# Performance work log

Hardware: AMD Instinct MI355X
Metric: run time of the kernel (lower is better)

Reference implementation:

```python
import jax, jax.numpy as jnp
import numpy as np

N_CRD = 32   # ceil(0.5 * 64) coordinate features
K = 16       # clus_val for knn
EPS = 1e-12


def _masked_dist(coords, mask):
    """Pairwise euclidean distances with padded/self pairs set to +inf.
    coords: [B,N,D], mask: [B,N] bool. Returns dist [B,N,N], valid [B,N,N]."""
    sq = jnp.sum(coords * coords, axis=-1)                 # [B,N]
    gram = jnp.einsum('bnd,bmd->bnm', coords, coords)      # [B,N,N]
    d2 = sq[:, :, None] + sq[:, None, :] - 2.0 * gram
    dist = jnp.sqrt(jnp.clip(d2, EPS, None))
    eye = jnp.eye(dist.shape[-1], dtype=bool)
    valid = (mask[:, :, None] & mask[:, None, :]) & ~eye   # fc adjmat, no self-loops
    dist = jnp.where(valid, dist, jnp.inf)                 # pad_val = +inf for eucl
    return dist, valid


def _knn(dist, k):
    """Boolean adjacency: True for the k smallest distances per row."""
    _, idx = jax.lax.top_k(-dist, k)                       # [B,N,K] nearest neighbours
    B, N, _ = dist.shape
    b = jnp.arange(B)[:, None, None]
    n = jnp.arange(N)[None, :, None]
    return jnp.zeros((B, N, N), bool).at[b, n, idx].set(True)


def setup_inputs() -> dict:
    key = jax.random.key(0)
    k1, k2 = jax.random.split(key)
    B, N, F = 64, 1024, 64
    nodes = jax.random.normal(k1, (B, N, F), jnp.float32)
    # realistic ragged graphs: each graph has between N/2 and N valid nodes
    lengths = jax.random.randint(k2, (B,), N // 2, N + 1)
    mask = jnp.arange(N)[None, :] < lengths[:, None]       # [B,N] bool
    return {"nodes": nodes, "mask": mask}


def reference(nodes, mask):
    coords = nodes[..., :N_CRD]
    dist, valid = _masked_dist(coords, mask)
    adjmat = _knn(dist, K) & valid                         # drop padded/self picks
    # dense analogue of distmat[new_adjmat].unsqueeze(-1): zeros off the adjacency
    new_edges = jnp.where(adjmat[..., None], dist[..., None], 0.0)  # [B,N,N,1]
    return new_edges, adjmat
```

## Files before the change

### kernel.cpp

```cpp
#include <hip/hip_runtime.h>
#include <math.h>

#define NROW 1024
#define INF_BITS 0x7F800000u
#define WINDOW   4.0e-3f
#define CLAMP_EPS 1e-12f

typedef float nf4 __attribute__((ext_vector_type(4)));

__device__ __forceinline__ unsigned long long ull_min(unsigned long long a, unsigned long long b) {
    return a < b ? a : b;
}
__device__ __forceinline__ unsigned umax2(unsigned a, unsigned b) { return a > b ? a : b; }

#define ROW_MINMAX(K, MN, MX)                                                           \
    {                                                                                   \
        MN = 0xFFFFFFFFu; MX = 0u;                                                      \
        _Pragma("unroll")                                                               \
        for (int tt = 0; tt < 16; ++tt) {                                               \
            const unsigned kk_ = K[tt];                                                 \
            MN = kk_ < MN ? kk_ : MN;                                                   \
            const unsigned kf_ = (kk_ < INF_BITS) ? kk_ : 0u;                           \
            MX = kf_ > MX ? kf_ : MX;                                                   \
        }                                                                               \
        _Pragma("unroll")                                                               \
        for (int d = 1; d < 64; d <<= 1) {                                              \
            const unsigned omn = (unsigned)__shfl_xor((int)MN, d);                      \
            const unsigned omx = (unsigned)__shfl_xor((int)MX, d);                      \
            MN = omn < MN ? omn : MN;                                                   \
            MX = omx > MX ? omx : MX;                                                   \
        }                                                                               \
    }

#define BISECT_STEP(K, LO, HI)                                                          \
    {                                                                                   \
        const unsigned mid_ = LO + ((HI - LO) >> 1);                                    \
        int cnt_ = 0;                                                                   \
        _Pragma("unroll")                                                               \
        for (int tt = 0; tt < 16; ++tt)                                                 \
            cnt_ += __popcll(__ballot(K[tt] < mid_));                                   \
        if (cnt_ >= 16) HI = mid_; else LO = mid_;                                      \
    }

#define RESOLVE_ROW(K, V, RLOC, SELOUT)                                                 \
    {                                                                                   \
        const float Vw = __uint_as_float(V) + WINDOW;                                   \
        int cS = 0, nE = 0, cW = 0;                                                     \
        unsigned ltm = 0u, eqm = 0u, cm = 0u;                                           \
        _Pragma("unroll")                                                               \
        for (int tt = 0; tt < 16; ++tt) {                                               \
            const unsigned kk_ = K[tt];                                                 \
            const bool l_ = kk_ < (V);                                                  \
            const bool e_ = kk_ == (V);                                                 \
            const bool c_ = __uint_as_float(kk_) <= Vw;                                 \
            cS += __popcll(__ballot(l_));                                               \
            nE += __popcll(__ballot(e_));                                               \
            cW += __popcll(__ballot(c_));                                               \
            ltm |= (l_ ? 1u : 0u) << tt;                                                \
            eqm |= (e_ ? 1u : 0u) << tt;                                                \
            cm  |= (c_ ? 1u : 0u) << tt;                                                \
        }                                                                               \
        if (cS + nE == 16 && cW == 16) {                                                \
            SELOUT = ltm | eqm;                                                         \
        } else {                                                                        \
            int myj = -1;                                                               \
            {                                                                           \
                int cum = 0;                                                            \
                _Pragma("unroll")                                                       \
                for (int tt = 0; tt < 16; ++tt) {                                       \
                    const unsigned long long bm = __ballot((cm >> tt) & 1u);            \
                    const int pc = __popcll(bm);                                        \
                    if (myj < 0 && lane >= cum && lane < cum + pc) {                    \
                        unsigned long long mm = bm;                                     \
                        for (int z = lane - cum; z > 0; --z) mm &= mm - 1ull;           \
                        myj = tt * 64 + (__ffsll((unsigned long long)mm) - 1);          \
                    }                                                                   \
                    cum += pc;                                                          \
                }                                                                       \
            }                                                                           \
            unsigned long long dbits = ~0ull;                                           \
            if (myj >= 0) {                                                             \
                const float4* cp = (const float4*)(nbase + (size_t)myj * 64);           \
                double sq_ = 0.0, dt_ = 0.0;                                            \
                _Pragma("unroll")                                                       \
                for (int f = 0; f < 8; ++f) {                                           \
                    const float4 v = cp[f];                                             \
                    const float4 a = rowc[(RLOC) * 8 + f];                              \
                    sq_ = fma((double)v.x, (double)v.x, sq_);                           \
                    sq_ = fma((double)v.y, (double)v.y, sq_);                           \
                    sq_ = fma((double)v.z, (double)v.z, sq_);                           \
                    sq_ = fma((double)v.w, (double)v.w, sq_);                           \
                    dt_ = fma((double)v.x, (double)a.x, dt_);                           \
                    dt_ = fma((double)v.y, (double)a.y, dt_);                           \
                    dt_ = fma((double)v.z, (double)a.z, dt_);                           \
                    dt_ = fma((double)v.w, (double)a.w, dt_);                           \
                }                                                                       \
                double d64 = fma(-2.0, dt_, sqr64[RLOC] + sq_);                         \
                d64 = fmax(d64, (double)CLAMP_EPS);                                     \
                dbits = (unsigned long long)__double_as_longlong(d64);                  \
            }                                                                           \
            unsigned selb = 0u;                                                         \
            bool act = (myj >= 0);                                                      \
            for (int round = 0; round < 16; ++round) {                                  \
                unsigned long long best = act ? dbits : ~0ull;                          \
                _Pragma("unroll")                                                       \
                for (int d = 1; d < 64; d <<= 1)                                        \
                    best = ull_min(best,                                                \
                        (unsigned long long)__shfl_xor((long long)best, d));            \
                int pj = (act && dbits == best) ? myj : 0x7FFFFFFF;                     \
                _Pragma("unroll")                                                       \
                for (int d = 1; d < 64; d <<= 1) {                                      \
                    const int o = __shfl_xor(pj, d);                                    \
                    pj = o < pj ? o : pj;                                               \
                }                                                                       \
                if (myj == pj) act = false;                                             \
                if (lane == (pj & 63)) selb |= 1u << (pj >> 6);                         \
            }                                                                           \
            SELOUT = selb;                                                              \
        }                                                                               \
    }

__global__ __launch_bounds__(256) void transpose_norm_kernel(
    const float* __restrict__ nodes, float4* __restrict__ wsT,
    float* __restrict__ sqc)
{
    const int w = blockIdx.x;
    const int l = (w & 7) * 32 + (w >> 3);
    const int g = l * 256 + threadIdx.x;
    const int b = g >> 10, j = g & 1023;
    const float4* cp = (const float4*)(nodes + (size_t)g * 64);
    float4 c[8];
    float s = 0.f;
#pragma unroll
    for (int f = 0; f < 8; ++f) {
        c[f] = cp[f];
        s = fmaf(c[f].x, c[f].x, s); s = fmaf(c[f].y, c[f].y, s);
        s = fmaf(c[f].z, c[f].z, s); s = fmaf(c[f].w, c[f].w, s);
    }
#pragma unroll
    for (int f = 0; f < 8; ++f)
        wsT[(((size_t)b * 8 + f) << 10) + j] = c[f];
    sqc[g] = s;
}

template <int USE_WS>
__global__ __launch_bounds__(64) void edge_knn_kernel(
    const float* __restrict__ nodes,
    const int*   __restrict__ mask,
    const float4* __restrict__ wsT,
    const float* __restrict__ sqcw,
    float*       __restrict__ out)
{
    const int lane = threadIdx.x;
    const int blk  = (int)((blockIdx.x & 7) * 2048 + (blockIdx.x >> 3));
    const int b    = blk >> 8;
    const int rowbase = (blk & 255) * 4;

    const int* maskb = mask + b * NROW;
    float* edges = out + (size_t)b * NROW * NROW;
    float* adjm  = out + (size_t)64 * NROW * NROW + (size_t)b * NROW * NROW;

    const int anyv = maskb[rowbase] | maskb[rowbase + 1] | maskb[rowbase + 2] | maskb[rowbase + 3];
    if (!anyv) {
        const nf4 z = {0.f, 0.f, 0.f, 0.f};
#pragma unroll
        for (int r = 0; r < 4; ++r) {
            nf4* e4 = reinterpret_cast<nf4*>(edges + (size_t)(rowbase + r) * NROW);
            nf4* a4 = reinterpret_cast<nf4*>(adjm  + (size_t)(rowbase + r) * NROW);
#pragma unroll
            for (int q = 0; q < 4; ++q) {
                __builtin_nontemporal_store(z, e4 + q * 64 + lane);
                __builtin_nontemporal_store(z, a4 + q * 64 + lane);
            }
        }
        return;
    }

    __shared__ float4 rowc[4 * 8];
    __shared__ float  sqr32s[4];
    __shared__ double sqr64[4];

    const float* nbase = nodes + (size_t)b * NROW * 64;

    if (lane < 32) {
        const int r = lane >> 3, f = lane & 7;
        rowc[lane] = ((const float4*)(nbase + (size_t)(rowbase + r) * 64))[f];
    }
    __syncthreads();
    if (lane < 4) {
        double s = 0.0;
#pragma unroll
        for (int f = 0; f < 8; ++f) {
            const float4 v = rowc[lane * 8 + f];
            s = fma((double)v.x, (double)v.x, s);
            s = fma((double)v.y, (double)v.y, s);
            s = fma((double)v.z, (double)v.z, s);
            s = fma((double)v.w, (double)v.w, s);
        }
        sqr64[lane] = s;
        sqr32s[lane] = (float)s;
    }
    __syncthreads();

    unsigned mb = 0u;
#pragma unroll
    for (int tt = 0; tt < 16; ++tt)
        mb |= (maskb[tt * 64 + lane] != 0 ? 1u : 0u) << tt;

    const int row0 = rowbase;
    const bool rv0 = maskb[row0 + 0] != 0;
    const bool rv1 = maskb[row0 + 1] != 0;
    const bool rv2 = maskb[row0 + 2] != 0;
    const bool rv3 = maskb[row0 + 3] != 0;
    const float sqr0 = sqr32s[0], sqr1 = sqr32s[1];
    const float sqr2 = sqr32s[2], sqr3 = sqr32s[3];

    unsigned k0[16], k1[16], k2[16], k3[16];

#pragma unroll
    for (int tt = 0; tt < 16; ++tt) {
        const int j = tt * 64 + lane;
        float4 c[8];
        float sA;
        if (USE_WS) {
            const float4* tbase = wsT + ((size_t)b * 8 << 10);
#pragma unroll
            for (int f = 0; f < 8; ++f) c[f] = tbase[(f << 10) + j];
            sA = sqcw[(size_t)b * NROW + j];
        } else {
            const float4* cp = (const float4*)(nbase + (size_t)j * 64);
#pragma unroll
            for (int f = 0; f < 8; ++f) c[f] = cp[f];
            sA = 0.f;
#pragma unroll
            for (int f = 0; f < 8; ++f) {
                sA = fmaf(c[f].x, c[f].x, sA); sA = fmaf(c[f].y, c[f].y, sA);
                sA = fmaf(c[f].z, c[f].z, sA); sA = fmaf(c[f].w, c[f].w, sA);
            }
        }

        float d0 = 0.f, d1 = 0.f, d2 = 0.f, d3 = 0.f;
#pragma unroll
        for (int f = 0; f < 8; ++f) {
            const float4 v  = c[f];
            const float4 a0 = rowc[0 * 8 + f];
            const float4 a1 = rowc[1 * 8 + f];
            const float4 a2 = rowc[2 * 8 + f];
            const float4 a3 = rowc[3 * 8 + f];
            d0 = fmaf(v.x, a0.x, d0); d0 = fmaf(v.y, a0.y, d0);
            d0 = fmaf(v.z, a0.z, d0); d0 = fmaf(v.w, a0.w, d0);
            d1 = fmaf(v.x, a1.x, d1); d1 = fmaf(v.y, a1.y, d1);
            d1 = fmaf(v.z, a1.z, d1); d1 = fmaf(v.w, a1.w, d1);
            d2 = fmaf(v.x, a2.x, d2); d2 = fmaf(v.y, a2.y, d2);
            d2 = fmaf(v.z, a2.z, d2); d2 = fmaf(v.w, a2.w, d2);
            d3 = fmaf(v.x, a3.x, d3); d3 = fmaf(v.y, a3.y, d3);
            d3 = fmaf(v.z, a3.z, d3); d3 = fmaf(v.w, a3.w, d3);
        }

        const bool cv = (mb >> tt) & 1u;
        float e_;
        e_ = fmaxf(fmaf(-2.f, d0, sqr0 + sA), CLAMP_EPS);
        k0[tt] = (cv && j != row0 + 0) ? __float_as_uint(e_) : INF_BITS;
        e_ = fmaxf(fmaf(-2.f, d1, sqr1 + sA), CLAMP_EPS);
        k1[tt] = (cv && j != row0 + 1) ? __float_as_uint(e_) : INF_BITS;
        e_ = fmaxf(fmaf(-2.f, d2, sqr2 + sA), CLAMP_EPS);
        k2[tt] = (cv && j != row0 + 2) ? __float_as_uint(e_) : INF_BITS;
        e_ = fmaxf(fmaf(-2.f, d3, sqr3 + sA), CLAMP_EPS);
        k3[tt] = (cv && j != row0 + 3) ? __float_as_uint(e_) : INF_BITS;
    }

    unsigned mn0, mx0, mn1, mx1, mn2, mx2, mn3, mx3;
    ROW_MINMAX(k0, mn0, mx0);
    ROW_MINMAX(k1, mn1, mx1);
    ROW_MINMAX(k2, mn2, mx2);
    ROW_MINMAX(k3, mn3, mx3);

    unsigned lo0 = mn0, hi0 = mx0 + 1u;
    unsigned lo1 = mn1, hi1 = mx1 + 1u;
    unsigned lo2 = mn2, hi2 = mx2 + 1u;
    unsigned lo3 = mn3, hi3 = mx3 + 1u;
    if (!rv0) { lo0 = 0u; hi0 = 1u; }
    if (!rv1) { lo1 = 0u; hi1 = 1u; }
    if (!rv2) { lo2 = 0u; hi2 = 1u; }
    if (!rv3) { lo3 = 0u; hi3 = 1u; }

    for (;;) {
        const unsigned dm = umax2(umax2(hi0 - lo0, hi1 - lo1), umax2(hi2 - lo2, hi3 - lo3));
        if (dm <= 1u) break;
        BISECT_STEP(k0, lo0, hi0);
        BISECT_STEP(k1, lo1, hi1);
        BISECT_STEP(k2, lo2, hi2);
        BISECT_STEP(k3, lo3, hi3);
    }

    unsigned sel0 = 0u, sel1 = 0u, sel2 = 0u, sel3 = 0u;
    if (rv0) RESOLVE_ROW(k0, lo0, 0, sel0);
    if (rv1) RESOLVE_ROW(k1, lo1, 1, sel1);
    if (rv2) RESOLVE_ROW(k2, lo2, 2, sel2);
    if (rv3) RESOLVE_ROW(k3, lo3, 3, sel3);

#pragma unroll
    for (int tt = 0; tt < 16; ++tt) {
        const int j = tt * 64 + lane;
        {
            const bool s = (sel0 >> tt) & 1u;
            __builtin_nontemporal_store(s ? sqrtf(__uint_as_float(k0[tt])) : 0.f,
                                        edges + (size_t)(row0 + 0) * NROW + j);
            __builtin_nontemporal_store(s ? 1.f : 0.f,
                                        adjm + (size_t)(row0 + 0) * NROW + j);
        }
        {
            const bool s = (sel1 >> tt) & 1u;
            __builtin_nontemporal_store(s ? sqrtf(__uint_as_float(k1[tt])) : 0.f,
                                        edges + (size_t)(row0 + 1) * NROW + j);
            __builtin_nontemporal_store(s ? 1.f : 0.f,
                                        adjm + (size_t)(row0 + 1) * NROW + j);
        }
        {
            const bool s = (sel2 >> tt) & 1u;
            __builtin_nontemporal_store(s ? sqrtf(__uint_as_float(k2[tt])) : 0.f,
                                        edges + (size_t)(row0 + 2) * NROW + j);
            __builtin_nontemporal_store(s ? 1.f : 0.f,
                                        adjm + (size_t)(row0 + 2) * NROW + j);
        }
        {
            const bool s = (sel3 >> tt) & 1u;
            __builtin_nontemporal_store(s ? sqrtf(__uint_as_float(k3[tt])) : 0.f,
                                        edges + (size_t)(row0 + 3) * NROW + j);
            __builtin_nontemporal_store(s ? 1.f : 0.f,
                                        adjm + (size_t)(row0 + 3) * NROW + j);
        }
    }
}

extern "C" void kernel_launch(void* const* d_in, const int* in_sizes, int n_in,
                              void* d_out, int out_size, void* d_ws, size_t ws_size,
                              hipStream_t stream)
{
    const float* nodes = (const float*)d_in[0];
    const int*   mask  = (const int*)d_in[1];
    float* out = (float*)d_out;

    dim3 grid(64 * 256);
    dim3 block(64);

    const size_t wsT_f4 = (size_t)64 * 8 * 1024;
    const size_t need   = wsT_f4 * sizeof(float4) + (size_t)64 * NROW * sizeof(float);
    const bool   use_ws = ws_size >= need;

    if (use_ws) {
        float4* wsT = (float4*)d_ws;
        float*  sqc = (float*)((char*)d_ws + wsT_f4 * sizeof(float4));
        hipLaunchKernelGGL(transpose_norm_kernel, dim3(64 * NROW / 256), dim3(256), 0, stream,
                           nodes, wsT, sqc);
        hipLaunchKernelGGL((edge_knn_kernel<1>), grid, block, 0, stream,
                           nodes, mask, (const float4*)wsT, (const float*)sqc, out);
    } else {
        hipLaunchKernelGGL((edge_knn_kernel<0>), grid, block, 0, stream,
                           nodes, mask, (const float4*)nullptr, (const float*)nullptr, out);
    }
}
```

Baseline: 291.7 us.

## Process two rows per wavefront with register-held query rows and skip masked column tiles

```diff
diff --git a/kernel.cpp b/kernel.cpp
--- a/kernel.cpp
+++ b/kernel.cpp
@@ -42,7 +42,7 @@
         if (cnt_ >= 16) HI = mid_; else LO = mid_;                                      \
     }
 
-#define RESOLVE_ROW(K, V, RLOC, SELOUT)                                                 \
+#define RESOLVE_ROW(K, V, RC, SQ64, SELOUT)                                             \
     {                                                                                   \
         const float Vw = __uint_as_float(V) + WINDOW;                                   \
         int cS = 0, nE = 0, cW = 0;                                                     \
@@ -85,7 +85,7 @@
                 _Pragma("unroll")                                                       \
                 for (int f = 0; f < 8; ++f) {                                           \
                     const float4 v = cp[f];                                             \
-                    const float4 a = rowc[(RLOC) * 8 + f];                              \
+                    const float4 a = RC[f];                                             \
                     sq_ = fma((double)v.x, (double)v.x, sq_);                           \
                     sq_ = fma((double)v.y, (double)v.y, sq_);                           \
                     sq_ = fma((double)v.z, (double)v.z, sq_);                           \
@@ -95,7 +95,7 @@
                     dt_ = fma((double)v.z, (double)a.z, dt_);                           \
                     dt_ = fma((double)v.w, (double)a.w, dt_);                           \
                 }                                                                       \
-                double d64 = fma(-2.0, dt_, sqr64[RLOC] + sq_);                         \
+                double d64 = fma(-2.0, dt_, (SQ64) + sq_);                              \
                 d64 = fmax(d64, (double)CLAMP_EPS);                                     \
                 dbits = (unsigned long long)__double_as_longlong(d64);                  \
             }                                                                           \
@@ -152,19 +152,19 @@
     float*       __restrict__ out)
 {
     const int lane = threadIdx.x;
-    const int blk  = (int)((blockIdx.x & 7) * 2048 + (blockIdx.x >> 3));
-    const int b    = blk >> 8;
-    const int rowbase = (blk & 255) * 4;
+    const int blk  = (int)((blockIdx.x & 7) * 4096 + (blockIdx.x >> 3));
+    const int b    = blk >> 9;
+    const int rowbase = (blk & 511) * 2;
 
     const int* maskb = mask + b * NROW;
     float* edges = out + (size_t)b * NROW * NROW;
     float* adjm  = out + (size_t)64 * NROW * NROW + (size_t)b * NROW * NROW;
 
-    const int anyv = maskb[rowbase] | maskb[rowbase + 1] | maskb[rowbase + 2] | maskb[rowbase + 3];
+    const int anyv = maskb[rowbase] | maskb[rowbase + 1];
     if (!anyv) {
         const nf4 z = {0.f, 0.f, 0.f, 0.f};
 #pragma unroll
-        for (int r = 0; r < 4; ++r) {
+        for (int r = 0; r < 2; ++r) {
             nf4* e4 = reinterpret_cast<nf4*>(edges + (size_t)(rowbase + r) * NROW);
             nf4* a4 = reinterpret_cast<nf4*>(adjm  + (size_t)(rowbase + r) * NROW);
 #pragma unroll
@@ -176,31 +176,34 @@
         return;
     }
 
-    __shared__ float4 rowc[4 * 8];
-    __shared__ float  sqr32s[4];
-    __shared__ double sqr64[4];
-
     const float* nbase = nodes + (size_t)b * NROW * 64;
 
-    if (lane < 32) {
-        const int r = lane >> 3, f = lane & 7;
-        rowc[lane] = ((const float4*)(nbase + (size_t)(rowbase + r) * 64))[f];
-    }
-    __syncthreads();
-    if (lane < 4) {
-        double s = 0.0;
-#pragma unroll
-        for (int f = 0; f < 8; ++f) {
-            const float4 v = rowc[lane * 8 + f];
-            s = fma((double)v.x, (double)v.x, s);
-            s = fma((double)v.y, (double)v.y, s);
-            s = fma((double)v.z, (double)v.z, s);
-            s = fma((double)v.w, (double)v.w, s);
-        }
-        sqr64[lane] = s;
-        sqr32s[lane] = (float)s;
-    }
-    __syncthreads();
+    float4 r0c[8], r1c[8];
+    {
+        const float4* rp0 = (const float4*)(nbase + (size_t)(rowbase + 0) * 64);
+        const float4* rp1 = (const float4*)(nbase + (size_t)(rowbase + 1) * 64);
+#pragma unroll
+        for (int f = 0; f < 8; ++f) { r0c[f] = rp0[f]; r1c[f] = rp1[f]; }
+    }
+    double sq64_0 = 0.0, sq64_1 = 0.0;
+#pragma unroll
+    for (int f = 0; f < 8; ++f) {
+        const float4 v = r0c[f];
+        sq64_0 = fma((double)v.x, (double)v.x, sq64_0);
+        sq64_0 = fma((double)v.y, (double)v.y, sq64_0);
+        sq64_0 = fma((double)v.z, (double)v.z, sq64_0);
+        sq64_0 = fma((double)v.w, (double)v.w, sq64_0);
+    }
+#pragma unroll
+    for (int f = 0; f < 8; ++f) {
+        const float4 v = r1c[f];
+        sq64_1 = fma((double)v.x, (double)v.x, sq64_1);
+        sq64_1 = fma((double)v.y, (double)v.y, sq64_1);
+        sq64_1 = fma((double)v.z, (double)v.z, sq64_1);
+        sq64_1 = fma((double)v.w, (double)v.w, sq64_1);
+    }
+    const float sqr0 = (float)sq64_0;
+    const float sqr1 = (float)sq64_1;
 
     unsigned mb = 0u;
 #pragma unroll
@@ -210,15 +213,15 @@
     const int row0 = rowbase;
     const bool rv0 = maskb[row0 + 0] != 0;
     const bool rv1 = maskb[row0 + 1] != 0;
-    const bool rv2 = maskb[row0 + 2] != 0;
-    const bool rv3 = maskb[row0 + 3] != 0;
-    const float sqr0 = sqr32s[0], sqr1 = sqr32s[1];
-    const float sqr2 = sqr32s[2], sqr3 = sqr32s[3];
-
-    unsigned k0[16], k1[16], k2[16], k3[16];
+
+    unsigned k0[16], k1[16];
 
 #pragma unroll
     for (int tt = 0; tt < 16; ++tt) {
+        if (__ballot((mb >> tt) & 1u) == 0ull) {
+            k0[tt] = INF_BITS; k1[tt] = INF_BITS;
+            continue;
+        }
         const int j = tt * 64 + lane;
         float4 c[8];
         float sA;
@@ -239,22 +242,16 @@
             }
         }
 
-        float d0 = 0.f, d1 = 0.f, d2 = 0.f, d3 = 0.f;
+        float d0 = 0.f, d1 = 0.f;
 #pragma unroll
         for (int f = 0; f < 8; ++f) {
             const float4 v  = c[f];
-            const float4 a0 = rowc[0 * 8 + f];
-            const float4 a1 = rowc[1 * 8 + f];
-            const float4 a2 = rowc[2 * 8 + f];
-            const float4 a3 = rowc[3 * 8 + f];
+            const float4 a0 = r0c[f];
+            const float4 a1 = r1c[f];
             d0 = fmaf(v.x, a0.x, d0); d0 = fmaf(v.y, a0.y, d0);
             d0 = fmaf(v.z, a0.z, d0); d0 = fmaf(v.w, a0.w, d0);
             d1 = fmaf(v.x, a1.x, d1); d1 = fmaf(v.y, a1.y, d1);
             d1 = fmaf(v.z, a1.z, d1); d1 = fmaf(v.w, a1.w, d1);
-            d2 = fmaf(v.x, a2.x, d2); d2 = fmaf(v.y, a2.y, d2);
-            d2 = fmaf(v.z, a2.z, d2); d2 = fmaf(v.w, a2.w, d2);
-            d3 = fmaf(v.x, a3.x, d3); d3 = fmaf(v.y, a3.y, d3);
-            d3 = fmaf(v.z, a3.z, d3); d3 = fmaf(v.w, a3.w, d3);
         }
 
         const bool cv = (mb >> tt) & 1u;
@@ -263,41 +260,27 @@
         k0[tt] = (cv && j != row0 + 0) ? __float_as_uint(e_) : INF_BITS;
         e_ = fmaxf(fmaf(-2.f, d1, sqr1 + sA), CLAMP_EPS);
         k1[tt] = (cv && j != row0 + 1) ? __float_as_uint(e_) : INF_BITS;
-        e_ = fmaxf(fmaf(-2.f, d2, sqr2 + sA), CLAMP_EPS);
-        k2[tt] = (cv && j != row0 + 2) ? __float_as_uint(e_) : INF_BITS;
-        e_ = fmaxf(fmaf(-2.f, d3, sqr3 + sA), CLAMP_EPS);
-        k3[tt] = (cv && j != row0 + 3) ? __float_as_uint(e_) : INF_BITS;
-    }
-
-    unsigned mn0, mx0, mn1, mx1, mn2, mx2, mn3, mx3;
+    }
+
+    unsigned mn0, mx0, mn1, mx1;
     ROW_MINMAX(k0, mn0, mx0);
     ROW_MINMAX(k1, mn1, mx1);
-    ROW_MINMAX(k2, mn2, mx2);
-    ROW_MINMAX(k3, mn3, mx3);
 
     unsigned lo0 = mn0, hi0 = mx0 + 1u;
     unsigned lo1 = mn1, hi1 = mx1 + 1u;
-    unsigned lo2 = mn2, hi2 = mx2 + 1u;
-    unsigned lo3 = mn3, hi3 = mx3 + 1u;
     if (!rv0) { lo0 = 0u; hi0 = 1u; }
     if (!rv1) { lo1 = 0u; hi1 = 1u; }
-    if (!rv2) { lo2 = 0u; hi2 = 1u; }
-    if (!rv3) { lo3 = 0u; hi3 = 1u; }
 
     for (;;) {
-        const unsigned dm = umax2(umax2(hi0 - lo0, hi1 - lo1), umax2(hi2 - lo2, hi3 - lo3));
+        const unsigned dm = umax2(hi0 - lo0, hi1 - lo1);
         if (dm <= 1u) break;
         BISECT_STEP(k0, lo0, hi0);
         BISECT_STEP(k1, lo1, hi1);
-        BISECT_STEP(k2, lo2, hi2);
-        BISECT_STEP(k3, lo3, hi3);
-    }
-
-    unsigned sel0 = 0u, sel1 = 0u, sel2 = 0u, sel3 = 0u;
-    if (rv0) RESOLVE_ROW(k0, lo0, 0, sel0);
-    if (rv1) RESOLVE_ROW(k1, lo1, 1, sel1);
-    if (rv2) RESOLVE_ROW(k2, lo2, 2, sel2);
-    if (rv3) RESOLVE_ROW(k3, lo3, 3, sel3);
+    }
+
+    unsigned sel0 = 0u, sel1 = 0u;
+    if (rv0) RESOLVE_ROW(k0, lo0, r0c, sq64_0, sel0);
+    if (rv1) RESOLVE_ROW(k1, lo1, r1c, sq64_1, sel1);
 
 #pragma unroll
     for (int tt = 0; tt < 16; ++tt) {
@@ -316,20 +299,6 @@
             __builtin_nontemporal_store(s ? 1.f : 0.f,
                                         adjm + (size_t)(row0 + 1) * NROW + j);
         }
-        {
-            const bool s = (sel2 >> tt) & 1u;
-            __builtin_nontemporal_store(s ? sqrtf(__uint_as_float(k2[tt])) : 0.f,
-                                        edges + (size_t)(row0 + 2) * NROW + j);
-            __builtin_nontemporal_store(s ? 1.f : 0.f,
-                                        adjm + (size_t)(row0 + 2) * NROW + j);
-        }
-        {
-            const bool s = (sel3 >> tt) & 1u;
-            __builtin_nontemporal_store(s ? sqrtf(__uint_as_float(k3[tt])) : 0.f,
-                                        edges + (size_t)(row0 + 3) * NROW + j);
-            __builtin_nontemporal_store(s ? 1.f : 0.f,
-                                        adjm + (size_t)(row0 + 3) * NROW + j);
-        }
     }
 }
 
@@ -341,7 +310,7 @@
     const int*   mask  = (const int*)d_in[1];
     float* out = (float*)d_out;
 
-    dim3 grid(64 * 256);
+    dim3 grid(64 * 512);
     dim3 block(64);
 
     const size_t wsT_f4 = (size_t)64 * 8 * 1024;
```

Measured after the change: 315.4 us. 1.08x slower.
